# Kernel optimization log

Measured on AMD Instinct MI355X. Metric: run time of the kernel, lower is better.

The kernel has to match this reference:

```python
import jax, jax.numpy as jnp
import numpy as np

B, C, H, W = 8, 256, 32, 32
N = H * W  # 1024; conv1 maps C -> N channels so all bmms are [B,N,N]


def setup_inputs() -> dict:
    key = jax.random.key(0)
    ks = jax.random.split(key, 11)
    s = 0.02  # weight scale to keep softmax logits in a sane range
    return {
        "x":     jax.random.normal(ks[0], (B, C, H, W), jnp.float32),
        "w1":    jax.random.normal(ks[1], (N, C), jnp.float32) * s,
        "b1":    jax.random.normal(ks[2], (N,), jnp.float32) * s,
        "wq":    jax.random.normal(ks[3], (N, N), jnp.float32) * s,
        "bq":    jax.random.normal(ks[4], (N,), jnp.float32) * s,
        "wv":    jax.random.normal(ks[5], (N, N), jnp.float32) * s,
        "bv":    jax.random.normal(ks[6], (N,), jnp.float32) * s,
        "w2":    jax.random.normal(ks[7], (C, N), jnp.float32) * s,
        "b2":    jax.random.normal(ks[8], (C,), jnp.float32) * s,
        "alpha": jax.random.normal(ks[9], (1,), jnp.float32),
        "beta":  jax.random.normal(ks[10], (1,), jnp.float32),
    }


def reference(x, w1, b1, wq, bq, wv, bv, w2, b2, alpha, beta):
    b, c, h, w = x.shape
    n = h * w
    # 1x1 convs as channel matmuls
    x1 = jnp.einsum('bchw,nc->bnhw', x, w1) + b1[None, :, None, None]  # [B,N,H,W]
    g = (jnp.einsum('bnhw,mn->bmhw', x1, wq) + bq[None, :, None, None]).reshape(b, n, n)
    r = (jnp.einsum('bnhw,mn->bmhw', x1, wv) + bv[None, :, None, None]).reshape(b, n, n)
    xf = x1.reshape(b, n, n)          # m^T in the torch code: [B, N_chan, HW]
    m = xf.transpose(0, 2, 1)         # m: [B, HW, N_chan]
    # spatial attention: z_s = softmax(m^T @ g)
    z_s = jax.nn.softmax(jnp.matmul(xf, g), axis=-1)            # [B,N,N]
    # channel attention: z_c = softmax(g^T @ m)
    z_c = jax.nn.softmax(jnp.matmul(g.transpose(0, 2, 1), m), axis=-1)  # [B,N,N]
    p_s = jnp.matmul(z_s, r)                                    # [B,N,HW]
    p_c = jnp.matmul(z_c, m).transpose(0, 2, 1)                 # [B,N,HW]
    p = (alpha[0] * p_s + beta[0] * p_c).reshape(b, n, h, w)
    out = jnp.einsum('bnhw,cn->bchw', p, w2) + b2[None, :, None, None]
    return out
```

## Files before the change

### kernel.cpp

```cpp
#include <hip/hip_runtime.h>
#include <hip/hip_bf16.h>


typedef __attribute__((ext_vector_type(4))) float f4;
typedef __attribute__((ext_vector_type(8))) short s8;
typedef __attribute__((ext_vector_type(4))) unsigned short us4;
typedef __attribute__((ext_vector_type(8))) unsigned short us8;

__device__ __forceinline__ unsigned short f2bf(float f) {
    __hip_bfloat16 h = __float2bfloat16(f);
    return __builtin_bit_cast(unsigned short, h);
}

#define GAS(p) ((const __attribute__((address_space(1))) unsigned int*)(p))
#define LAS(p) ((__attribute__((address_space(3))) unsigned int*)(p))

__global__ __launch_bounds__(256) void conv_weights(
    const float* __restrict__ w1, const float* __restrict__ wq,
    const float* __restrict__ wv, const float* __restrict__ w2,
    unsigned short* __restrict__ w1b, unsigned short* __restrict__ wqb,
    unsigned short* __restrict__ wvb, unsigned short* __restrict__ w2b,
    const float* __restrict__ bq, const float* __restrict__ bv,
    float* __restrict__ biasqv)
{
    long i = (long)blockIdx.x * 256 + threadIdx.x;
    if (i >= 655360) {
        long j = i - 655360;
        if (j < 512) {
            f4 v = (j < 256) ? ((const f4*)bq)[j] : ((const f4*)bv)[j - 256];
            ((f4*)biasqv)[j] = v;
        }
        return;
    }
    const float* src; unsigned short* dst; long base;
    if (i < 65536)               { src = w1; dst = w1b; base = 0; }
    else if (i < 65536+262144)   { src = wq; dst = wqb; base = 65536; }
    else if (i < 65536+524288)   { src = wv; dst = wvb; base = 65536+262144; }
    else                         { src = w2; dst = w2b; base = 65536+524288; }
    long j = i - base;
    f4 v = ((const f4*)src)[j];
    us4 o;
    #pragma unroll
    for (int k = 0; k < 4; ++k) o[k] = f2bf(v[k]);
    ((us4*)dst)[j] = o;
}

__global__ __launch_bounds__(256) void transpose_x(
    const float* __restrict__ x, unsigned short* __restrict__ xT)
{
    __shared__ float tl[32][33];
    const int b  = blockIdx.z;
    const int q0 = blockIdx.x * 32;
    const int c0 = blockIdx.y * 32;
    const int tx = threadIdx.x & 31, ty = threadIdx.x >> 5;
    #pragma unroll
    for (int j = 0; j < 4; ++j)
        tl[ty + j*8][tx] = x[((long)(b*256 + c0 + ty + j*8))*1024 + q0 + tx];
    __syncthreads();
    #pragma unroll
    for (int j = 0; j < 4; ++j)
        xT[((long)(b*1024 + q0 + ty + j*8))*256 + c0 + tx] = f2bf(tl[tx][ty + j*8]);
}

template<int BIAS, int OUTF32, int SPLIT, int NPASS>
__global__ __launch_bounds__(512, 2) void gemm256(
    const unsigned short* __restrict__ A0, const unsigned short* __restrict__ Bt0,
    const unsigned short* __restrict__ A1, const unsigned short* __restrict__ Bt1,
    long sA, long sB, int lda, int ldb,
    void* __restrict__ Cv0, void* __restrict__ Cv1, long sC, int ldc,
    const float* __restrict__ bias, int nt1)
{
    __shared__ __align__(16) unsigned short As[3][16384];
    __shared__ __align__(16) unsigned short Bs[3][8192];

    const int gx = gridDim.x, gy = gridDim.y;
    const int nwg = gx * gy * gridDim.z;
    int d = blockIdx.x + gx * (blockIdx.y + gy * blockIdx.z);
    int swz = (d & 7) * (nwg >> 3) + (d >> 3);
    const int bx = swz % gx; int tq = swz / gx;
    const int by = tq % gy;  const int bz = tq / gy;

    const int b  = bz;
    const int m0 = by * 256;
    const int n0 = bx * 128;
    const int t  = threadIdx.x;
    const int w  = t >> 6, l = t & 63;
    const int wr = w >> 1, wc = w & 1;
    const int lr = l & 15, lg = l >> 4;

    const unsigned short* A0b = A0  + (long)b * sA;
    const unsigned short* B0b = Bt0 + (long)b * sB;
    const unsigned short* A1b = (NPASS > 1) ? A1  + (long)b * sA : nullptr;
    const unsigned short* B1b = (NPASS > 1) ? Bt1 + (long)b * sB : nullptr;

    const int rl  = l >> 3;
    const int gsw = ((l & 7) ^ (rl & 7)) * 8;

    const int NT = NPASS * nt1;

    auto stageA = [&](int sp, int bf) {
        const unsigned short* Ap = A0b; int kt = sp * 64;
        if (NPASS > 1 && sp >= nt1) { Ap = A1b; kt = (sp - nt1) * 64; }
        #pragma unroll
        for (int i = 0; i < 4; ++i) {
            const int rb = w*32 + i*8;
            __builtin_amdgcn_global_load_lds(GAS(Ap + (long)(m0 + rb + rl)*lda + kt + gsw),
                                             LAS(&As[bf][rb*64]), 16, 0, 0);
        }
    };
    auto stageB = [&](int sp, int bf) {
        const unsigned short* Bp = B0b; int kt = sp * 64;
        if (NPASS > 1 && sp >= nt1) { Bp = B1b; kt = (sp - nt1) * 64; }
        #pragma unroll
        for (int i = 0; i < 2; ++i) {
            const int rb = w*16 + i*8;
            __builtin_amdgcn_global_load_lds(GAS(Bp + (long)(n0 + rb + rl)*ldb + kt + gsw),
                                             LAS(&Bs[bf][rb*64]), 16, 0, 0);
        }
    };

    f4 acc[4][4];
    #pragma unroll
    for (int i = 0; i < 4; ++i)
        #pragma unroll
        for (int j = 0; j < 4; ++j) acc[i][j] = (f4){0.f, 0.f, 0.f, 0.f};

    stageA(0, 0); stageB(0, 0);
    stageA(1, 1); stageB(1, 1);
    asm volatile("s_waitcnt vmcnt(6)" ::: "memory");
    __builtin_amdgcn_sched_barrier(0);
    __builtin_amdgcn_s_barrier();

    s8 a0[4], b0[4], a1f[4], b1f[4];

    #pragma unroll
    for (int m = 0; m < 4; ++m) {
        const int R = wr*64 + m*16 + lr;
        a0[m] = *(const s8*)&As[0][R*64 + ((lg ^ (R & 7)) * 8)];
    }
    #pragma unroll
    for (int n = 0; n < 4; ++n) {
        const int R = wc*64 + n*16 + lr;
        b0[n] = *(const s8*)&Bs[0][R*64 + ((lg ^ (R & 7)) * 8)];
    }
    asm volatile("s_waitcnt lgkmcnt(0)" ::: "memory");
    __builtin_amdgcn_sched_barrier(0);

    int buf = 0;
    for (int s = 0; s < NT; ++s) {
        int bn = buf + 2; if (bn >= 3) bn -= 3;
        int bx1 = buf + 1; if (bx1 >= 3) bx1 -= 3;

        #pragma unroll
        for (int m = 0; m < 4; ++m) {
            const int R = wr*64 + m*16 + lr;
            a1f[m] = *(const s8*)&As[buf][R*64 + (((4 + lg) ^ (R & 7)) * 8)];
        }
        #pragma unroll
        for (int n = 0; n < 4; ++n) {
            const int R = wc*64 + n*16 + lr;
            b1f[n] = *(const s8*)&Bs[buf][R*64 + (((4 + lg) ^ (R & 7)) * 8)];
        }
        if (s + 2 < NT) stageA(s + 2, bn);
        __builtin_amdgcn_s_setprio(1);
        #pragma unroll
        for (int m = 0; m < 4; ++m)
            #pragma unroll
            for (int n = 0; n < 4; ++n)
                acc[m][n] = __builtin_amdgcn_mfma_f32_16x16x32_bf16(a0[m], b0[n], acc[m][n], 0, 0, 0);
        __builtin_amdgcn_s_setprio(0);
        asm volatile("s_waitcnt lgkmcnt(0)" ::: "memory");
        __builtin_amdgcn_sched_barrier(0);

        if (s + 1 < NT) {
            if (s + 2 < NT) asm volatile("s_waitcnt vmcnt(4)" ::: "memory");
            else            asm volatile("s_waitcnt vmcnt(0)" ::: "memory");
            __builtin_amdgcn_sched_barrier(0);
            __builtin_amdgcn_s_barrier();
            #pragma unroll
            for (int m = 0; m < 4; ++m) {
                const int R = wr*64 + m*16 + lr;
                a0[m] = *(const s8*)&As[bx1][R*64 + ((lg ^ (R & 7)) * 8)];
            }
            #pragma unroll
            for (int n = 0; n < 4; ++n) {
                const int R = wc*64 + n*16 + lr;
                b0[n] = *(const s8*)&Bs[bx1][R*64 + ((lg ^ (R & 7)) * 8)];
            }
            if (s + 2 < NT) stageB(s + 2, bn);
            __builtin_amdgcn_s_setprio(1);
            #pragma unroll
            for (int m = 0; m < 4; ++m)
                #pragma unroll
                for (int n = 0; n < 4; ++n)
                    acc[m][n] = __builtin_amdgcn_mfma_f32_16x16x32_bf16(a1f[m], b1f[n], acc[m][n], 0, 0, 0);
            __builtin_amdgcn_s_setprio(0);
            asm volatile("s_waitcnt lgkmcnt(0)" ::: "memory");
            __builtin_amdgcn_sched_barrier(0);
        } else {
            __builtin_amdgcn_s_setprio(1);
            #pragma unroll
            for (int m = 0; m < 4; ++m)
                #pragma unroll
                for (int n = 0; n < 4; ++n)
                    acc[m][n] = __builtin_amdgcn_mfma_f32_16x16x32_bf16(a1f[m], b1f[n], acc[m][n], 0, 0, 0);
            __builtin_amdgcn_s_setprio(0);
        }

        buf = bx1;
    }

    void* Cd = Cv0; int nbase = n0;
    if (SPLIT && n0 >= 1024) { Cd = Cv1; nbase = n0 - 1024; }

    const int rbase = lg * 4;
    #pragma unroll
    for (int m = 0; m < 4; ++m) {
        #pragma unroll
        for (int n = 0; n < 4; ++n) {
            const int row  = m0 + wr*64 + m*16 + rbase;
            const int col  = nbase + wc*64 + n*16 + lr;
            const int bcol = n0    + wc*64 + n*16 + lr;
            #pragma unroll
            for (int j = 0; j < 4; ++j) {
                float v = acc[m][n][j];
                if (BIAS == 1) v += bias[row + j];
                else if (BIAS == 2) v += bias[bcol];
                const long idx = (long)b*sC + (long)(row + j)*ldc + col;
                if (OUTF32) ((float*)Cd)[idx] = v;
                else ((unsigned short*)Cd)[idx] = f2bf(v);
            }
        }
    }
}

template<int BIAS, int OUTF32, int NT1, int NBUF>
__global__ __launch_bounds__(256) void gemm_pipe(
    const unsigned short* __restrict__ A0, const unsigned short* __restrict__ Bt0,
    long sA, long sB, int lda, int ldb,
    void* __restrict__ Cv0, long sC, int ldc,
    const float* __restrict__ bias)
{
    constexpr int NT = NT1;
    __shared__ __align__(16) unsigned short As[NBUF][4096];
    __shared__ __align__(16) unsigned short Bs[NBUF][4096];

    const int gx = gridDim.x, gy = gridDim.y;
    const int nwg = gx * gy * gridDim.z;
    int d = blockIdx.x + gx * (blockIdx.y + gy * blockIdx.z);
    int swz = (d & 7) * (nwg >> 3) + (d >> 3);
    const int bx = swz % gx; int tq = swz / gx;
    const int by = tq % gy;  const int bz = tq / gy;

    const int b  = bz;
    const int m0 = by * 128;
    const int n0 = bx * 128;
    const int t  = threadIdx.x;
    const int w  = t >> 6, l = t & 63;
    const int wr = w >> 1, wc = w & 1;
    const int lr = l & 15;

    const unsigned short* A0b = A0  + (long)b * sA;
    const unsigned short* B0b = Bt0 + (long)b * sB;

    const int rA   = w*32 + (l >> 2);
    const int cswz = ((l & 3) ^ ((l >> 3) & 3)) * 8;
    const int swzr = (((l >> 4) ^ ((lr >> 1) & 3)) * 8);

    f4 acc[4][4];
    #pragma unroll
    for (int i = 0; i < 4; ++i)
        #pragma unroll
        for (int j = 0; j < 4; ++j) acc[i][j] = (f4){0.f, 0.f, 0.f, 0.f};

    auto stage = [&](int sp, int bf) {
        const int kt = sp * 32;
        __builtin_amdgcn_global_load_lds(GAS(A0b + (long)(m0 + rA     )*lda + kt + cswz), LAS(&As[bf][w*1024      ]), 16, 0, 0);
        __builtin_amdgcn_global_load_lds(GAS(A0b + (long)(m0 + rA + 16)*lda + kt + cswz), LAS(&As[bf][w*1024 + 512]), 16, 0, 0);
        __builtin_amdgcn_global_load_lds(GAS(B0b + (long)(n0 + rA     )*ldb + kt + cswz), LAS(&Bs[bf][w*1024      ]), 16, 0, 0);
        __builtin_amdgcn_global_load_lds(GAS(B0b + (long)(n0 + rA + 16)*ldb + kt + cswz), LAS(&Bs[bf][w*1024 + 512]), 16, 0, 0);
    };

    #pragma unroll
    for (int dpl = 0; dpl < NBUF - 1; ++dpl) stage(dpl, dpl);

    int buf = 0;
    for (int s = 0; s < NT; ++s) {
        if (NBUF >= 4 && s + 2 < NT) asm volatile("s_waitcnt vmcnt(8)" ::: "memory");
        else if (s + 1 < NT)         asm volatile("s_waitcnt vmcnt(4)" ::: "memory");
        else                         asm volatile("s_waitcnt vmcnt(0)" ::: "memory");
        __builtin_amdgcn_s_barrier();
        __builtin_amdgcn_sched_barrier(0);

        s8 aF[4], bF[4];
        #pragma unroll
        for (int m = 0; m < 4; ++m) aF[m] = *(const s8*)&As[buf][(wr*64 + m*16 + lr)*32 + swzr];
        #pragma unroll
        for (int n = 0; n < 4; ++n) bF[n] = *(const s8*)&Bs[buf][(wc*64 + n*16 + lr)*32 + swzr];

        if (s + NBUF - 1 < NT) {
            int bn = buf + NBUF - 1; if (bn >= NBUF) bn -= NBUF;
            stage(s + NBUF - 1, bn);
        }

        __builtin_amdgcn_s_setprio(1);
        #pragma unroll
        for (int m = 0; m < 4; ++m)
            #pragma unroll
            for (int n = 0; n < 4; ++n)
                acc[m][n] = __builtin_amdgcn_mfma_f32_16x16x32_bf16(aF[m], bF[n], acc[m][n], 0, 0, 0);
        __builtin_amdgcn_s_setprio(0);

        if (++buf == NBUF) buf = 0;
    }

    const int rbase = (l >> 4) * 4;
    #pragma unroll
    for (int m = 0; m < 4; ++m) {
        #pragma unroll
        for (int n = 0; n < 4; ++n) {
            const int row = m0 + wr*64 + m*16 + rbase;
            const int col = n0 + wc*64 + n*16 + lr;
            #pragma unroll
            for (int j = 0; j < 4; ++j) {
                float v = acc[m][n][j];
                if (BIAS == 1) v += bias[row + j];
                else if (BIAS == 2) v += bias[col];
                const long idx = (long)b*sC + (long)(row + j)*ldc + col;
                if (OUTF32) ((float*)Cv0)[idx] = v;
                else ((unsigned short*)Cv0)[idx] = f2bf(v);
            }
        }
    }
}

__global__ __launch_bounds__(256) void row_softmax(
    const float* __restrict__ S, unsigned short* __restrict__ Z,
    const float* __restrict__ scale_p)
{
    const int wid = threadIdx.x >> 6, l = threadIdx.x & 63;
    const long row = (long)blockIdx.x * 4 + wid;
    const float* src = S + row * 1024;
    f4 v[4];
    #pragma unroll
    for (int i = 0; i < 4; ++i) v[i] = *(const f4*)&src[(i*64 + l)*4];
    float m = -3.4e38f;
    #pragma unroll
    for (int i = 0; i < 4; ++i)
        #pragma unroll
        for (int j = 0; j < 4; ++j) m = fmaxf(m, v[i][j]);
    #pragma unroll
    for (int off = 32; off; off >>= 1) m = fmaxf(m, __shfl_xor(m, off));
    float s = 0.f;
    #pragma unroll
    for (int i = 0; i < 4; ++i)
        #pragma unroll
        for (int j = 0; j < 4; ++j) { v[i][j] = __expf(v[i][j] - m); s += v[i][j]; }
    #pragma unroll
    for (int off = 32; off; off >>= 1) s += __shfl_xor(s, off);
    const float c = scale_p[0] / s;
    #pragma unroll
    for (int i = 0; i < 4; ++i) {
        us4 o;
        #pragma unroll
        for (int j = 0; j < 4; ++j) o[j] = f2bf(v[i][j] * c);
        *(us4*)&Z[row*1024 + (long)(i*64 + l)*4] = o;
    }
}

__global__ __launch_bounds__(256) void col_stats(
    const float* __restrict__ S, float* __restrict__ cm, float* __restrict__ cs)
{
    __shared__ float pm[4][64], ps[4][64];
    const int b  = blockIdx.y;
    const int ci = threadIdx.x & 63, ks = threadIdx.x >> 6;
    const int q  = blockIdx.x * 64 + ci;
    const float* Sb = S + (long)b * 1048576 + q;
    float m = -3.4e38f, s = 0.f;
    for (int k = ks*256; k < ks*256 + 256; ++k) {
        float v = Sb[(long)k * 1024];
        float dlt = v - m;
        float ed = __expf(-fabsf(dlt));
        if (dlt > 0.f) { s = s * ed + 1.f; m = v; } else s += ed;
    }
    pm[ks][ci] = m; ps[ks][ci] = s;
    __syncthreads();
    if (threadIdx.x < 64) {
        float M = pm[0][ci];
        #pragma unroll
        for (int i = 1; i < 4; ++i) M = fmaxf(M, pm[i][ci]);
        float Ssum = 0.f;
        #pragma unroll
        for (int i = 0; i < 4; ++i) Ssum += ps[i][ci] * __expf(pm[i][ci] - M);
        cm[b*1024 + q] = M;
        cs[b*1024 + q] = Ssum;
    }
}

__global__ __launch_bounds__(256) void col_write(
    const float* __restrict__ S, const float* __restrict__ cm,
    const float* __restrict__ cs, unsigned short* __restrict__ Z,
    const float* __restrict__ scale_p)
{
    __shared__ float tile[64][65];
    const int b  = blockIdx.z;
    const int q0 = blockIdx.x * 64;
    const int k0 = blockIdx.y * 64;
    const int t  = threadIdx.x;
    const float* Sb = S + (long)b * 1048576;
    const int tq = t & 15, tr = t >> 4;
    #pragma unroll
    for (int ii = 0; ii < 4; ++ii) {
        const int kr = tr + ii*16;
        f4 v = *(const f4*)&Sb[(long)(k0 + kr)*1024 + q0 + tq*4];
        tile[kr][tq*4+0] = v[0]; tile[kr][tq*4+1] = v[1];
        tile[kr][tq*4+2] = v[2]; tile[kr][tq*4+3] = v[3];
    }
    __syncthreads();
    const int qr = t >> 2, kp = t & 3;
    const int q = q0 + qr;
    const float m   = cm[b*1024 + q];
    const float inv = scale_p[0] / cs[b*1024 + q];
    unsigned short* Zb = Z + (long)b*1048576 + (long)q*1024 + k0 + kp*16;
    us8 o0, o1;
    #pragma unroll
    for (int e = 0; e < 8; ++e) o0[e] = f2bf(inv * __expf(tile[kp*16 + e][qr] - m));
    #pragma unroll
    for (int e = 0; e < 8; ++e) o1[e] = f2bf(inv * __expf(tile[kp*16 + 8 + e][qr] - m));
    *(us8*)&Zb[0] = o0;
    *(us8*)&Zb[8] = o1;
}

extern "C" void kernel_launch(void* const* d_in, const int* in_sizes, int n_in,
                              void* d_out, int out_size, void* d_ws, size_t ws_size,
                              hipStream_t stream)
{
    const float* x     = (const float*)d_in[0];
    const float* w1    = (const float*)d_in[1];
    const float* b1    = (const float*)d_in[2];
    const float* wq    = (const float*)d_in[3];
    const float* bq    = (const float*)d_in[4];
    const float* wv    = (const float*)d_in[5];
    const float* bv    = (const float*)d_in[6];
    const float* w2    = (const float*)d_in[7];
    const float* b2    = (const float*)d_in[8];
    const float* alpha = (const float*)d_in[9];
    const float* beta  = (const float*)d_in[10];
    float* out = (float*)d_out;

    char* ws = (char*)d_ws;
    size_t off = 0;
    auto alloc = [&](size_t bytes) -> void* {
        void* p = ws + off; off += (bytes + 255) & ~(size_t)255; return p;
    };
    unsigned short* w1b   = (unsigned short*)alloc(1024L*256*2);
    unsigned short* wqvb  = (unsigned short*)alloc(2048L*1024*2);
    unsigned short* w2b   = (unsigned short*)alloc(256L*1024*2);
    float*          biasqv= (float*)alloc(2048L*4);
    float*          cmv   = (float*)alloc(8L*1024*4);
    float*          csv   = (float*)alloc(8L*1024*4);
    unsigned short* xTb   = (unsigned short*)alloc(8L*1024*256*2);
    unsigned short* x1b   = (unsigned short*)alloc(8L*1024*1024*2);
    unsigned short* x1tb  = (unsigned short*)alloc(8L*1024*1024*2);
    unsigned short* gtb   = (unsigned short*)alloc(8L*1024*1024*2);
    unsigned short* rtb   = (unsigned short*)alloc(8L*1024*1024*2);
    float*          Sf    = (float*)alloc(8L*1024*1024*4);
    unsigned short* zsb = x1tb;
    unsigned short* zcb = gtb;
    unsigned short* Ptb = (unsigned short*)Sf;

    const long S1M = 1048576;

    conv_weights<<<2562, 256, 0, stream>>>(w1, wq, wv, w2, w1b, wqvb, wqvb + S1M, w2b, bq, bv, biasqv);
    transpose_x<<<dim3(32, 8, 8), 256, 0, stream>>>(x, xTb);

    gemm256<1,0,0,1><<<dim3(8, 4, 8), 512, 0, stream>>>(
        w1b, xTb, nullptr, nullptr, 0, 262144, 256, 256, x1b, nullptr, S1M, 1024, b1, 4);
    gemm256<2,0,0,1><<<dim3(8, 32, 1), 512, 0, stream>>>(
        xTb, w1b, nullptr, nullptr, 0, 0, 256, 256, x1tb, nullptr, 0, 1024, b1, 4);
    gemm256<2,0,1,1><<<dim3(16, 32, 1), 512, 0, stream>>>(
        x1tb, wqvb, nullptr, nullptr, 0, 0, 1024, 1024, gtb, rtb, 0, 1024, biasqv, 16);
    gemm256<0,1,0,1><<<dim3(8, 4, 8), 512, 0, stream>>>(
        x1b, gtb, nullptr, nullptr, S1M, S1M, 1024, 1024, Sf, nullptr, S1M, 1024, nullptr, 16);
    row_softmax<<<2048, 256, 0, stream>>>(Sf, zsb, alpha);
    col_stats<<<dim3(16, 8), 256, 0, stream>>>(Sf, cmv, csv);
    col_write<<<dim3(16, 16, 8), 256, 0, stream>>>(Sf, cmv, csv, zcb, beta);
    gemm256<0,0,0,2><<<dim3(8, 4, 8), 512, 0, stream>>>(
        rtb, zsb, zcb, x1b, S1M, S1M, 1024, 1024, Ptb, nullptr, S1M, 1024, nullptr, 16);
    gemm_pipe<1,1,32,4><<<dim3(8, 2, 8), 256, 0, stream>>>(
        w2b, Ptb, 0, S1M, 1024, 1024, out, 262144, 1024, b2);
}
```

Baseline: 180.4 us.

## Use a 256x256-tile ping-pong pipelined GEMM for the fused Q/V projection

Adds a new gemm8p kernel for the x1^T times [wq;wv] projection. It uses 256x256 output tiles, split K-halves, and a double-buffered LDS layout. An eight-phase schedule interleaves LDS fragment reads, async global-to-LDS loads and MFMA blocks, with explicit barriers and waitcnts. The larger tile halves the block count and raises operand reuse per loaded byte. The risk is one block per CU with heavier registers, and a simple scalar bf16 epilogue.

```diff
diff --git a/kernel.cpp b/kernel.cpp
--- a/kernel.cpp
+++ b/kernel.cpp
@@ -60,6 +60,142 @@
     #pragma unroll
     for (int j = 0; j < 4; ++j)
         xT[((long)(b*1024 + q0 + ty + j*8))*256 + c0 + tx] = f2bf(tl[tx][ty + j*8]);
+}
+
+template<int BIAS, int SPLIT>
+__global__ __launch_bounds__(512, 2) void gemm8p(
+    const unsigned short* __restrict__ A0, const unsigned short* __restrict__ Bt0,
+    int lda, int ldb,
+    void* __restrict__ Cv0, void* __restrict__ Cv1, int ldc,
+    const float* __restrict__ bias)
+{
+    constexpr int NT = 16;
+    __shared__ __align__(16) unsigned short As[2][2][8192];
+    __shared__ __align__(16) unsigned short Bs[2][2][8192];
+
+    const int gx = gridDim.x, gy = gridDim.y;
+    const int nwg = gx * gy;
+    int d = blockIdx.x + gx * blockIdx.y;
+    int swz = (d & 7) * (nwg >> 3) + (d >> 3);
+    const int bx = swz % gx;
+    const int by = swz / gx;
+
+    const int m0 = by * 256;
+    const int n0 = bx * 256;
+    const int t  = threadIdx.x;
+    const int w  = t >> 6, l = t & 63;
+    const int wr = w >> 2, wc = w & 3;
+    const int lr = l & 15, lg = l >> 4;
+
+    const unsigned short* Asrc = A0  + (long)m0 * lda;
+    const unsigned short* Bsrc = Bt0 + (long)n0 * ldb;
+
+    const int rl4 = l >> 2;
+    const int gsw = ((l & 3) ^ ((l >> 3) & 3)) * 8;
+    const int rsw = (lr >> 1) & 3;
+
+    auto stage = [&](const unsigned short* src, int ld_, unsigned short* slot,
+                     int sp, int kh) {
+        #pragma unroll
+        for (int i = 0; i < 2; ++i) {
+            const int rb = i*128 + w*16;
+            __builtin_amdgcn_global_load_lds(
+                GAS(src + (long)(rb + rl4)*ld_ + sp*64 + kh*32 + gsw),
+                LAS(slot + rb*32), 16, 0, 0);
+        }
+    };
+
+    f4 acc[8][4];
+    #pragma unroll
+    for (int i = 0; i < 8; ++i)
+        #pragma unroll
+        for (int j = 0; j < 4; ++j) acc[i][j] = (f4){0.f, 0.f, 0.f, 0.f};
+
+    s8 aF[4], bF[4];
+    auto rdA = [&](int db, int kh, int mh) {
+        #pragma unroll
+        for (int m = 0; m < 4; ++m) {
+            const int R = wr*128 + mh*64 + m*16 + lr;
+            aF[m] = *(const s8*)&As[db][kh][R*32 + ((lg ^ rsw) * 8)];
+        }
+    };
+    auto rdB = [&](int db, int kh) {
+        #pragma unroll
+        for (int n = 0; n < 4; ++n) {
+            const int R = wc*64 + n*16 + lr;
+            bF[n] = *(const s8*)&Bs[db][kh][R*32 + ((lg ^ rsw) * 8)];
+        }
+    };
+
+#define MM8(MH)                                                                  \
+    __builtin_amdgcn_s_setprio(1);                                               \
+    _Pragma("unroll")                                                            \
+    for (int m_ = 0; m_ < 4; ++m_)                                               \
+        _Pragma("unroll")                                                        \
+        for (int n_ = 0; n_ < 4; ++n_)                                           \
+            acc[(MH)*4 + m_][n_] = __builtin_amdgcn_mfma_f32_16x16x32_bf16(      \
+                aF[m_], bF[n_], acc[(MH)*4 + m_][n_], 0, 0, 0);                  \
+    __builtin_amdgcn_s_setprio(0);
+
+#define PH8(DB, KH, MH, RB, STG, VM)                                             \
+    rdA(DB, KH, MH);                                                             \
+    if (RB) rdB(DB, KH);                                                         \
+    STG;                                                                         \
+    __builtin_amdgcn_sched_barrier(0);                                           \
+    __builtin_amdgcn_s_barrier();                                                \
+    asm volatile("s_waitcnt lgkmcnt(0)" ::: "memory");                           \
+    __builtin_amdgcn_sched_barrier(0);                                           \
+    MM8(MH);                                                                     \
+    VM;                                                                          \
+    __builtin_amdgcn_s_barrier();
+
+    stage(Asrc, lda, &As[0][0][0], 0, 0);
+    stage(Bsrc, ldb, &Bs[0][0][0], 0, 0);
+    stage(Asrc, lda, &As[0][1][0], 0, 1);
+    stage(Bsrc, ldb, &Bs[0][1][0], 0, 1);
+    stage(Asrc, lda, &As[1][0][0], 1, 0);
+    stage(Bsrc, ldb, &Bs[1][0][0], 1, 0);
+    asm volatile("s_waitcnt vmcnt(4)" ::: "memory");
+    __builtin_amdgcn_sched_barrier(0);
+    __builtin_amdgcn_s_barrier();
+
+    for (int j = 0; j < NT/2; ++j) {
+        const int tb = 2*j + 1;
+        const int t2 = (2*j + 2) & (NT - 1);
+        const int t3 = (2*j + 3) & (NT - 1);
+        PH8(0,0,0, 1, stage(Asrc, lda, &As[1][1][0], tb, 1), (void)0)
+        PH8(0,0,1, 0, stage(Bsrc, ldb, &Bs[1][1][0], tb, 1), (void)0)
+        PH8(0,1,0, 1, stage(Asrc, lda, &As[0][0][0], t2, 0), (void)0)
+        PH8(0,1,1, 0, stage(Bsrc, ldb, &Bs[0][0][0], t2, 0),
+            asm volatile("s_waitcnt vmcnt(4)" ::: "memory"))
+        PH8(1,0,0, 1, stage(Asrc, lda, &As[0][1][0], t2, 1), (void)0)
+        PH8(1,0,1, 0, stage(Bsrc, ldb, &Bs[0][1][0], t2, 1), (void)0)
+        PH8(1,1,0, 1, stage(Asrc, lda, &As[1][0][0], t3, 0), (void)0)
+        PH8(1,1,1, 0, stage(Bsrc, ldb, &Bs[1][0][0], t3, 0),
+            asm volatile("s_waitcnt vmcnt(4)" ::: "memory"))
+    }
+#undef PH8
+#undef MM8
+
+    void* Cd = Cv0; int nbase = n0;
+    if (SPLIT && n0 >= 1024) { Cd = Cv1; nbase = n0 - 1024; }
+
+    const int rbase = lg * 4;
+    #pragma unroll
+    for (int mi = 0; mi < 8; ++mi) {
+        #pragma unroll
+        for (int n = 0; n < 4; ++n) {
+            const int row  = m0 + wr*128 + mi*16 + rbase;
+            const int col  = nbase + wc*64 + n*16 + lr;
+            const int bcol = n0    + wc*64 + n*16 + lr;
+            #pragma unroll
+            for (int j = 0; j < 4; ++j) {
+                float v = acc[mi][n][j];
+                if (BIAS == 2) v += bias[bcol];
+                ((unsigned short*)Cd)[(long)(row + j)*ldc + col] = f2bf(v);
+            }
+        }
+    }
 }
 
 template<int BIAS, int OUTF32, int SPLIT, int NPASS>
@@ -478,8 +614,8 @@
         w1b, xTb, nullptr, nullptr, 0, 262144, 256, 256, x1b, nullptr, S1M, 1024, b1, 4);
     gemm256<2,0,0,1><<<dim3(8, 32, 1), 512, 0, stream>>>(
         xTb, w1b, nullptr, nullptr, 0, 0, 256, 256, x1tb, nullptr, 0, 1024, b1, 4);
-    gemm256<2,0,1,1><<<dim3(16, 32, 1), 512, 0, stream>>>(
-        x1tb, wqvb, nullptr, nullptr, 0, 0, 1024, 1024, gtb, rtb, 0, 1024, biasqv, 16);
+    gemm8p<2,1><<<dim3(8, 32), 512, 0, stream>>>(
+        x1tb, wqvb, 1024, 1024, gtb, rtb, 1024, biasqv);
     gemm256<0,1,0,1><<<dim3(8, 4, 8), 512, 0, stream>>>(
         x1b, gtb, nullptr, nullptr, S1M, S1M, 1024, 1024, Sf, nullptr, S1M, 1024, nullptr, 16);
     row_softmax<<<2048, 256, 0, stream>>>(Sf, zsb, alpha);
```

After: 175.8 us. -2.6%, faster.
